# Kernel optimization log

Hardware: AMD Instinct MI355X
Metric: run time of the kernel (lower is better)

Reference implementation:

```python
import jax, jax.numpy as jnp
import numpy as np

B, N, M = 32, 512, 512
EPS = 0.05        # Sinkhorn entropic regularization (approximates exact EMD flow)
N_ITERS = 50      # fixed Sinkhorn iterations
NEG = -1e9        # log(0) surrogate for masked particles


def setup_inputs() -> dict:
    key = jax.random.key(0)
    k1, k2, k3, k4, k5, k6 = jax.random.split(key, 6)
    a_mask = (jax.random.uniform(k1, (B, N)) > 0.1).astype(jnp.float32)
    b_mask = (jax.random.uniform(k2, (B, M)) > 0.1).astype(jnp.float32)
    a_mask = a_mask.at[:, 0].set(1.0)  # guarantee nonempty clouds
    b_mask = b_mask.at[:, 0].set(1.0)
    pc_a = jnp.concatenate([jax.random.normal(k3, (B, N, 2)),
                            jax.random.uniform(k5, (B, N, 1), minval=0.1, maxval=1.0)], axis=-1)
    pc_b = jnp.concatenate([jax.random.normal(k4, (B, M, 2)),
                            jax.random.uniform(k6, (B, M, 1), minval=0.1, maxval=1.0)], axis=-1)
    return {"a_mask": a_mask, "pc_a": pc_a, "b_mask": b_mask, "pc_b": pc_b}


def _sinkhorn_logflow(loga, logb, logK):
    # log-domain Sinkhorn: find P with row sums exp(loga), col sums exp(logb)
    def body(i, carry):
        logu, logv = carry
        logu = loga - jax.scipy.special.logsumexp(logK + logv[:, None, :], axis=2)
        logv = logb - jax.scipy.special.logsumexp(logK + logu[:, :, None], axis=1)
        return (logu, logv)
    logu = jnp.zeros_like(loga)
    logv = jnp.zeros_like(logb)
    logu, logv = jax.lax.fori_loop(0, N_ITERS, body, (logu, logv))
    return logu[:, :, None] + logK + logv[:, None, :]  # [B, N, M]


def _emd_flow(a_pt, b_pt, dist, va, vb):
    # normalized pt distributions (emd(..., norm=True))
    aw = a_pt / jnp.sum(a_pt, axis=-1, keepdims=True)
    bw = b_pt / jnp.sum(b_pt, axis=-1, keepdims=True)
    loga = jnp.where(va, jnp.log(jnp.where(va, aw, 1.0)), NEG)
    logb = jnp.where(vb, jnp.log(jnp.where(vb, bw, 1.0)), NEG)
    logK = -dist / EPS
    flow = jnp.exp(_sinkhorn_logflow(loga, logb, logK))
    return flow * va[:, :, None].astype(flow.dtype) * vb[:, None, :].astype(flow.dtype)


def reference(a_mask, pc_a, b_mask, pc_b):
    a_pt = a_mask * pc_a[..., -1]              # [B, N]
    b_pt = b_mask * pc_b[..., -1]              # [B, M]
    va = a_pt > 0
    vb = b_pt > 0
    # masked pairwise (eta, phi) distance matrix
    diff = pc_a[:, :, None, :2] - pc_b[:, None, :, :2]      # [B, N, M, 2]
    d = jnp.sqrt(jnp.sum(diff * diff, axis=-1) + 1e-12)
    dist = d * va[:, :, None].astype(d.dtype) * vb[:, None, :].astype(d.dtype)
    # optimal-transport flow (detached in the original: computed on CPU numpy)
    flow = jax.lax.stop_gradient(_emd_flow(a_pt, b_pt, dist, va, vb))
    ot_term = jnp.sum(dist * dist * flow, axis=(-1, -2))    # [B]
    # huber_loss(reduction='none'), delta=1
    e = a_pt.sum(axis=-1) - b_pt.sum(axis=-1)
    huber = jnp.where(jnp.abs(e) <= 1.0, 0.5 * e * e, jnp.abs(e) - 0.5)
    return ot_term + huber
```

## Files before the change

kernel.cpp:

```cpp
#include <hip/hip_runtime.h>
#include <math.h>

#define NB 32
#define NP 512
#define RG 8
#define RPB 64
#define ITERS 50
#define EPSV   0.05f
#define INVEPS 20.0f

typedef unsigned long long u64;
typedef unsigned int u32;

#define N_PACK (2*NB*RG*NP)

__device__ __forceinline__ void st32(u32* p, u32 v) {
  __hip_atomic_store(p, v, __ATOMIC_RELAXED, __HIP_MEMORY_SCOPE_AGENT);
}
__device__ __forceinline__ u32 ld32(const u32* p) {
  return __hip_atomic_load(p, __ATOMIC_RELAXED, __HIP_MEMORY_SCOPE_AGENT);
}
__device__ __forceinline__ void st64f(float2* p, float tag, float val) {
  union { float2 f; u64 u; } c; c.f = make_float2(tag, val);
  __hip_atomic_store((u64*)p, c.u, __ATOMIC_RELAXED, __HIP_MEMORY_SCOPE_AGENT);
}
__device__ __forceinline__ float2 ld64f(const float2* p) {
  union { u64 u; float2 f; } c;
  c.u = __hip_atomic_load((const u64*)p, __ATOMIC_RELAXED, __HIP_MEMORY_SCOPE_AGENT);
  return c.f;
}

__device__ __forceinline__ u32 tag_of(int k) {
  return (0x765431u >> (4 * (k % 6))) & 0xFu;
}
__device__ __forceinline__ u32 pack_slot(float v, u32 tag) {
  return (__float_as_uint(v) & ~7u) | tag;
}

__global__ __launch_bounds__(NP) void emd_kernel(
    const float* __restrict__ a_mask, const float* __restrict__ pc_a,
    const float* __restrict__ b_mask, const float* __restrict__ pc_b,
    u32* __restrict__ pack, float2* __restrict__ epi,
    float* __restrict__ out)
{
  const int rb = blockIdx.x;
  const int b  = rb >> 3;
  const int rg = rb & 7;
  const int t  = threadIdx.x;
  const int chunk = t & 7;
  const int lrow  = t >> 3;
  const int grow  = rg*RPB + lrow;
  const int lane  = t & 63, wid = t >> 6;

  __shared__ __align__(16) float rho_l[NP];
  __shared__ __align__(16) float bw_l[NP];
  __shared__ __align__(16) float u_l[RPB];
  __shared__ __align__(16) float sm[NP];
  __shared__ float red[16];

  float4 eKreg[16];
  float  eKcol[RPB];
  float  aw_r, bw_t, hub = 0.f;

  {
    const float apt = a_mask[b*NP+t] * pc_a[((size_t)b*NP+t)*3+2];
    const float bpt = b_mask[b*NP+t] * pc_b[((size_t)b*NP+t)*3+2];
    float ra = apt, rv = bpt;
    #pragma unroll
    for (int o = 32; o; o >>= 1) { ra += __shfl_xor(ra, o); rv += __shfl_xor(rv, o); }
    if (lane == 0) { red[wid] = ra; red[8+wid] = rv; }
    __syncthreads();
    float asum = 0.f, bsum = 0.f;
    #pragma unroll
    for (int w = 0; w < 8; ++w) { asum += red[w]; bsum += red[8+w]; }
    const float e = asum - bsum, ae = fabsf(e);
    hub = (ae <= 1.f) ? 0.5f*e*e : (ae - 0.5f);
    sm[t]   = (apt > 0.f) ? apt/asum : 0.f;
    bw_l[t] = (bpt > 0.f) ? bpt/bsum : 0.f;
    __syncthreads();
    aw_r = sm[grow];
    bw_t = bw_l[t];
    const float ax = pc_a[((size_t)b*NP+grow)*3+0];
    const float ay = pc_a[((size_t)b*NP+grow)*3+1];
    const bool  va = aw_r > 0.f;
    #pragma unroll
    for (int cc = 0; cc < 16; ++cc) {
      float r[4];
      #pragma unroll
      for (int e2 = 0; e2 < 4; ++e2) {
        const int col = 32*cc + 4*chunk + e2;
        const float bx = pc_b[((size_t)b*NP+col)*3+0];
        const float by = pc_b[((size_t)b*NP+col)*3+1];
        const bool  vb = bw_l[col] > 0.f;
        const float dx = ax-bx, dy = ay-by;
        const float d  = sqrtf(dx*dx + dy*dy + 1e-12f);
        r[e2] = (va && vb) ? __expf((-INVEPS)*d) : 1.f;
      }
      eKreg[cc] = make_float4(r[0], r[1], r[2], r[3]);
    }
    const float bx0 = pc_b[((size_t)b*NP+t)*3+0];
    const float by0 = pc_b[((size_t)b*NP+t)*3+1];
    const bool  vb0 = bw_t > 0.f;
    #pragma unroll
    for (int i = 0; i < RPB; ++i) {
      const int row = rg*RPB + i;
      const float axi = pc_a[((size_t)b*NP+row)*3+0];
      const float ayi = pc_a[((size_t)b*NP+row)*3+1];
      const bool  vai = sm[row] > 0.f;
      const float dx = axi-bx0, dy = ayi-by0;
      const float d  = sqrtf(dx*dx + dy*dy + 1e-12f);
      eKcol[i] = (vai && vb0) ? __expf((-INVEPS)*d) : 1.f;
    }
    rho_l[t] = 1.f;
    __syncthreads();
  }

  for (int k = 1; k <= ITERS; ++k) {
    const u32 tag = tag_of(k);
    const int par = k & 1;
    const u32* base = pack + ((size_t)par*NB + b)*RG*NP + t;

    {
      const float4* r4p = (const float4*)rho_l;
      float dot = 0.f;
      #pragma unroll
      for (int cc = 0; cc < 16; ++cc) {
        const float4 g4 = r4p[8*cc + chunk];
        const float4 kk = eKreg[cc];
        dot += kk.x*g4.x + kk.y*g4.y + kk.z*g4.z + kk.w*g4.w;
      }
      #pragma unroll
      for (int o = 4; o; o >>= 1) dot += __shfl_xor(dot, o);
      if (chunk == 0) u_l[lrow] = aw_r / fmaxf(dot, 1e-38f);
    }
    __syncthreads();

    float sc_own;
    {
      const float4* u4p = (const float4*)u_l;
      float sc = 0.f;
      #pragma unroll
      for (int i4 = 0; i4 < 16; ++i4) {
        const float4 uu = u4p[i4];
        sc += eKcol[4*i4+0]*uu.x + eKcol[4*i4+1]*uu.y
            + eKcol[4*i4+2]*uu.z + eKcol[4*i4+3]*uu.w;
      }
      sc_own = sc;
      st32(pack + (((size_t)par*NB + b)*RG + rg)*NP + t, pack_slot(sc, tag));
    }

    u32 q[RG];
    #pragma unroll
    for (int r = 0; r < RG; ++r)
      if (r != rg) q[r] = ld32(base + (size_t)r*NP);

    {
      unsigned pend = 0xFFu & ~(1u << rg);
      long long sweeps = 0;
      while (true) {
        unsigned np = 0;
        #pragma unroll
        for (int r = 0; r < RG; ++r)
          if ((pend >> r) & 1u)
            if ((q[r] & 7u) != tag) np |= (1u << r);
        pend = np;
        if (!pend) break;
        #pragma unroll
        for (int r = 0; r < RG; ++r)
          if ((pend >> r) & 1u)
            q[r] = ld32(base + (size_t)r*NP);
        if (++sweeps > (1LL<<24)) break;
      }
      float S = sc_own;
      #pragma unroll
      for (int r = 0; r < RG; ++r)
        if (r != rg) S += __uint_as_float(q[r]);
      rho_l[t] = bw_t / fmaxf(S, 1e-38f);
    }
    __syncthreads();
  }

  float acc = 0.f;
  {
    const float ur = u_l[lrow];
    const float4* r4p = (const float4*)rho_l;
    #pragma unroll
    for (int cc = 0; cc < 16; ++cc) {
      const float4 g4 = r4p[8*cc + chunk];
      const float4 kk = eKreg[cc];
      const float ek[4] = {kk.x, kk.y, kk.z, kk.w};
      const float vv[4] = {g4.x, g4.y, g4.z, g4.w};
      #pragma unroll
      for (int e2 = 0; e2 < 4; ++e2) {
        const float lk = __logf(fmaxf(ek[e2], 1e-38f));
        const float d2 = (EPSV*lk)*(EPSV*lk);
        const float v  = d2 * ur * ek[e2] * vv[e2];
        acc += (ek[e2] > 0.f) ? v : 0.f;
      }
    }
  }
  sm[t] = acc;
  __syncthreads();
  if (t < 64) {
    float v = 0.f;
    #pragma unroll
    for (int q2 = 0; q2 < 8; ++q2) v += sm[t*8+q2];
    #pragma unroll
    for (int o = 32; o; o >>= 1) v += __shfl_xor(v, o);
    if (t == 0) st64f(epi + (size_t)b*RG + rg, 51.f, v);
  }
  if (rg == 0 && t < RG) {
    float2 pr;
    long long spins = 0;
    do {
      pr = ld64f(epi + (size_t)b*RG + t);
      if (pr.x == 51.f) break;
      __builtin_amdgcn_s_sleep(1);
    } while (++spins < (1LL<<27));
    float v = pr.y;
    #pragma unroll
    for (int o = 4; o; o >>= 1) v += __shfl_xor(v, o);
    if (t == 0) out[b] = v + hub;
  }
}

extern "C" void kernel_launch(void* const* d_in, const int* in_sizes, int n_in,
                              void* d_out, int out_size, void* d_ws, size_t ws_size,
                              hipStream_t stream) {
  const float* a_mask = (const float*)d_in[0];
  const float* pc_a   = (const float*)d_in[1];
  const float* b_mask = (const float*)d_in[2];
  const float* pc_b   = (const float*)d_in[3];
  float* out = (float*)d_out;
  u32*    pack = (u32*)d_ws;
  float2* epi  = (float2*)(pack + N_PACK);
  (void)in_sizes; (void)n_in; (void)out_size; (void)ws_size;

  emd_kernel<<<NB*RG, NP, 0, stream>>>(a_mask, pc_a, b_mask, pc_b,
                                       pack, epi, out);
}
```

Before: 196.1 us.

## Process two batches per block with 16 row groups to overlap cross-block exchange

Adds a new kernel in which each block handles two batch elements (X and Y) interleaved, with each batch split across 16 blocks of 32 rows instead of 8 blocks of 64. The Y half's compute is issued while the X half's cross-block partial sums are in flight, hiding the spin-wait latency of the inter-block reduction. Spin loops also add s_sleep backoff. The old kernel is kept as a fallback when the workspace is too small. Twice as many exchange partners per batch raises the polling traffic, and the extra register arrays may cause spilling.

```diff
diff --git a/kernel.cpp b/kernel.cpp
--- a/kernel.cpp
+++ b/kernel.cpp
@@ -3,16 +3,21 @@
 
 #define NB 32
 #define NP 512
-#define RG 8
-#define RPB 64
 #define ITERS 50
 #define EPSV   0.05f
 #define INVEPS 20.0f
 
+#define NPAIR 16
+#define GG 16
+#define RPB2 32
+#define PAR_STRIDE2 (NPAIR*2*GG*NP)
+#define N_PACK2 (2*PAR_STRIDE2)
+#define RG 8
+#define RPB 64
+#define N_PACK (2*NB*RG*NP)
+
 typedef unsigned long long u64;
 typedef unsigned int u32;
-
-#define N_PACK (2*NB*RG*NP)
 
 __device__ __forceinline__ void st32(u32* p, u32 v) {
   __hip_atomic_store(p, v, __ATOMIC_RELAXED, __HIP_MEMORY_SCOPE_AGENT);
@@ -37,7 +42,335 @@
   return (__float_as_uint(v) & ~7u) | tag;
 }
 
-__global__ __launch_bounds__(NP) void emd_kernel(
+__global__ __launch_bounds__(NP, 2) void emd_pair_kernel(
+    const float* __restrict__ a_mask, const float* __restrict__ pc_a,
+    const float* __restrict__ b_mask, const float* __restrict__ pc_b,
+    u32* __restrict__ pack, float2* __restrict__ epi,
+    float* __restrict__ out)
+{
+  const int rb = blockIdx.x;
+  const int p  = rb >> 4;
+  const int g  = rb & 15;
+  const int X  = 2*p, Y = 2*p + 1;
+  const int t  = threadIdx.x;
+  const int chunk = t & 15;
+  const int lrow  = t >> 4;
+  const int grow  = g*RPB2 + lrow;
+  const int lane  = t & 63, wid = t >> 6;
+
+  __shared__ __align__(16) float rhoX_l[NP], rhoY_l[NP];
+  __shared__ __align__(16) float bwX_l[NP],  bwY_l[NP];
+  __shared__ __align__(16) float uX_l[RPB2], uY_l[RPB2];
+  __shared__ __align__(16) float sm[NP];
+  __shared__ float red[32];
+
+  float4 eKregX[8], eKregY[8];
+  float  eKcolX[RPB2], eKcolY[RPB2];
+  float  aw_rX, bw_tX, hubX;
+  float  aw_rY, bw_tY, hubY;
+
+  u32* ownX = pack + ((size_t)(X*GG + g))*NP + t;
+  u32* ownY = pack + ((size_t)(Y*GG + g))*NP + t;
+  const u32* baseX = pack + (size_t)X*GG*NP + t;
+  const u32* baseY = pack + (size_t)Y*GG*NP + t;
+
+  const float aptX = a_mask[X*NP+t] * pc_a[((size_t)X*NP+t)*3+2];
+  const float bptX = b_mask[X*NP+t] * pc_b[((size_t)X*NP+t)*3+2];
+  const float aptY = a_mask[Y*NP+t] * pc_a[((size_t)Y*NP+t)*3+2];
+  const float bptY = b_mask[Y*NP+t] * pc_b[((size_t)Y*NP+t)*3+2];
+  {
+    float r0 = aptX, r1 = bptX, r2 = aptY, r3 = bptY;
+    #pragma unroll
+    for (int o = 32; o; o >>= 1) {
+      r0 += __shfl_xor(r0, o); r1 += __shfl_xor(r1, o);
+      r2 += __shfl_xor(r2, o); r3 += __shfl_xor(r3, o);
+    }
+    if (lane == 0) { red[wid]=r0; red[8+wid]=r1; red[16+wid]=r2; red[24+wid]=r3; }
+    __syncthreads();
+    float asX=0.f, bsX=0.f, asY=0.f, bsY=0.f;
+    #pragma unroll
+    for (int w = 0; w < 8; ++w) {
+      asX += red[w]; bsX += red[8+w]; asY += red[16+w]; bsY += red[24+w];
+    }
+    const float eX = asX - bsX, aeX = fabsf(eX);
+    hubX = (aeX <= 1.f) ? 0.5f*eX*eX : (aeX - 0.5f);
+    const float eY = asY - bsY, aeY = fabsf(eY);
+    hubY = (aeY <= 1.f) ? 0.5f*eY*eY : (aeY - 0.5f);
+    sm[t]    = (aptX > 0.f) ? aptX/asX : 0.f;
+    bwX_l[t] = (bptX > 0.f) ? bptX/bsX : 0.f;
+    bwY_l[t] = (bptY > 0.f) ? bptY/bsY : 0.f;
+    __syncthreads();
+    aw_rX = sm[grow]; bw_tX = bwX_l[t]; bw_tY = bwY_l[t];
+    {
+      const float ax = pc_a[((size_t)X*NP+grow)*3+0];
+      const float ay = pc_a[((size_t)X*NP+grow)*3+1];
+      const bool  va = aw_rX > 0.f;
+      #pragma unroll
+      for (int cc = 0; cc < 8; ++cc) {
+        float r[4];
+        #pragma unroll
+        for (int e2 = 0; e2 < 4; ++e2) {
+          const int col = 64*cc + 4*chunk + e2;
+          const float bx = pc_b[((size_t)X*NP+col)*3+0];
+          const float by = pc_b[((size_t)X*NP+col)*3+1];
+          const bool  vb = bwX_l[col] > 0.f;
+          const float dx = ax-bx, dy = ay-by;
+          const float d  = sqrtf(dx*dx + dy*dy + 1e-12f);
+          r[e2] = (va && vb) ? __expf((-INVEPS)*d) : 1.f;
+        }
+        eKregX[cc] = make_float4(r[0], r[1], r[2], r[3]);
+      }
+      const float bx0 = pc_b[((size_t)X*NP+t)*3+0];
+      const float by0 = pc_b[((size_t)X*NP+t)*3+1];
+      const bool  vb0 = bw_tX > 0.f;
+      #pragma unroll
+      for (int i = 0; i < RPB2; ++i) {
+        const int row = g*RPB2 + i;
+        const float axi = pc_a[((size_t)X*NP+row)*3+0];
+        const float ayi = pc_a[((size_t)X*NP+row)*3+1];
+        const bool  vai = sm[row] > 0.f;
+        const float dx = axi-bx0, dy = ayi-by0;
+        const float d  = sqrtf(dx*dx + dy*dy + 1e-12f);
+        eKcolX[i] = (vai && vb0) ? __expf((-INVEPS)*d) : 1.f;
+      }
+    }
+    rhoX_l[t] = 1.f;
+    __syncthreads();
+    sm[t] = (aptY > 0.f) ? aptY/asY : 0.f;
+    __syncthreads();
+    aw_rY = sm[grow];
+    {
+      const float ax = pc_a[((size_t)Y*NP+grow)*3+0];
+      const float ay = pc_a[((size_t)Y*NP+grow)*3+1];
+      const bool  va = aw_rY > 0.f;
+      #pragma unroll
+      for (int cc = 0; cc < 8; ++cc) {
+        float r[4];
+        #pragma unroll
+        for (int e2 = 0; e2 < 4; ++e2) {
+          const int col = 64*cc + 4*chunk + e2;
+          const float bx = pc_b[((size_t)Y*NP+col)*3+0];
+          const float by = pc_b[((size_t)Y*NP+col)*3+1];
+          const bool  vb = bwY_l[col] > 0.f;
+          const float dx = ax-bx, dy = ay-by;
+          const float d  = sqrtf(dx*dx + dy*dy + 1e-12f);
+          r[e2] = (va && vb) ? __expf((-INVEPS)*d) : 1.f;
+        }
+        eKregY[cc] = make_float4(r[0], r[1], r[2], r[3]);
+      }
+      const float bx0 = pc_b[((size_t)Y*NP+t)*3+0];
+      const float by0 = pc_b[((size_t)Y*NP+t)*3+1];
+      const bool  vb0 = bw_tY > 0.f;
+      #pragma unroll
+      for (int i = 0; i < RPB2; ++i) {
+        const int row = g*RPB2 + i;
+        const float axi = pc_a[((size_t)Y*NP+row)*3+0];
+        const float ayi = pc_a[((size_t)Y*NP+row)*3+1];
+        const bool  vai = sm[row] > 0.f;
+        const float dx = axi-bx0, dy = ayi-by0;
+        const float d  = sqrtf(dx*dx + dy*dy + 1e-12f);
+        eKcolY[i] = (vai && vb0) ? __expf((-INVEPS)*d) : 1.f;
+      }
+    }
+    rhoY_l[t] = 1.f;
+    __syncthreads();
+  }
+
+  for (int k = 1; k <= ITERS; ++k) {
+    const u32 tag = tag_of(k);
+    const size_t po = (size_t)(k & 1) * (size_t)PAR_STRIDE2;
+
+    {
+      const float4* r4p = (const float4*)rhoX_l;
+      float dot = 0.f;
+      #pragma unroll
+      for (int cc = 0; cc < 8; ++cc) {
+        const float4 g4 = r4p[16*cc + chunk];
+        const float4 kk = eKregX[cc];
+        dot += kk.x*g4.x + kk.y*g4.y + kk.z*g4.z + kk.w*g4.w;
+      }
+      #pragma unroll
+      for (int o = 8; o; o >>= 1) dot += __shfl_xor(dot, o);
+      if (chunk == 0) uX_l[lrow] = aw_rX / fmaxf(dot, 1e-38f);
+    }
+    __syncthreads();
+
+    float scoX;
+    {
+      const float4* u4p = (const float4*)uX_l;
+      float sc = 0.f;
+      #pragma unroll
+      for (int i4 = 0; i4 < 8; ++i4) {
+        const float4 uu = u4p[i4];
+        sc += eKcolX[4*i4+0]*uu.x + eKcolX[4*i4+1]*uu.y
+            + eKcolX[4*i4+2]*uu.z + eKcolX[4*i4+3]*uu.w;
+      }
+      scoX = sc;
+      st32(ownX + po, pack_slot(sc, tag));
+    }
+    u32 qx[GG];
+    #pragma unroll
+    for (int r = 0; r < GG; ++r)
+      if (r != g) qx[r] = ld32(baseX + po + (size_t)r*NP);
+    asm volatile("" ::: "memory");
+
+    {
+      const float4* r4p = (const float4*)rhoY_l;
+      float dot = 0.f;
+      #pragma unroll
+      for (int cc = 0; cc < 8; ++cc) {
+        const float4 g4 = r4p[16*cc + chunk];
+        const float4 kk = eKregY[cc];
+        dot += kk.x*g4.x + kk.y*g4.y + kk.z*g4.z + kk.w*g4.w;
+      }
+      #pragma unroll
+      for (int o = 8; o; o >>= 1) dot += __shfl_xor(dot, o);
+      if (chunk == 0) uY_l[lrow] = aw_rY / fmaxf(dot, 1e-38f);
+    }
+    __syncthreads();
+
+    float scoY;
+    {
+      const float4* u4p = (const float4*)uY_l;
+      float sc = 0.f;
+      #pragma unroll
+      for (int i4 = 0; i4 < 8; ++i4) {
+        const float4 uu = u4p[i4];
+        sc += eKcolY[4*i4+0]*uu.x + eKcolY[4*i4+1]*uu.y
+            + eKcolY[4*i4+2]*uu.z + eKcolY[4*i4+3]*uu.w;
+      }
+      scoY = sc;
+      st32(ownY + po, pack_slot(sc, tag));
+    }
+    u32 qy[GG];
+    #pragma unroll
+    for (int r = 0; r < GG; ++r)
+      if (r != g) qy[r] = ld32(baseY + po + (size_t)r*NP);
+    asm volatile("" ::: "memory");
+
+    {
+      unsigned pend = 0xFFFFu & ~(1u << g);
+      int sweeps = 0;
+      while (true) {
+        unsigned np = 0;
+        #pragma unroll
+        for (int r = 0; r < GG; ++r)
+          if ((pend >> r) & 1u)
+            if ((qx[r] & 7u) != tag) np |= (1u << r);
+        pend = np;
+        if (!pend) break;
+        #pragma unroll
+        for (int r = 0; r < GG; ++r)
+          if ((pend >> r) & 1u)
+            qx[r] = ld32(baseX + po + (size_t)r*NP);
+        ++sweeps;
+        if (sweeps > 64) __builtin_amdgcn_s_sleep(1);
+        if (sweeps > (1<<16)) break;
+      }
+      float S = scoX;
+      #pragma unroll
+      for (int r = 0; r < GG; ++r)
+        if (r != g) S += __uint_as_float(qx[r]);
+      rhoX_l[t] = bw_tX / fmaxf(S, 1e-38f);
+    }
+
+    {
+      unsigned pend = 0xFFFFu & ~(1u << g);
+      int sweeps = 0;
+      while (true) {
+        unsigned np = 0;
+        #pragma unroll
+        for (int r = 0; r < GG; ++r)
+          if ((pend >> r) & 1u)
+            if ((qy[r] & 7u) != tag) np |= (1u << r);
+        pend = np;
+        if (!pend) break;
+        #pragma unroll
+        for (int r = 0; r < GG; ++r)
+          if ((pend >> r) & 1u)
+            qy[r] = ld32(baseY + po + (size_t)r*NP);
+        ++sweeps;
+        if (sweeps > 64) __builtin_amdgcn_s_sleep(1);
+        if (sweeps > (1<<16)) break;
+      }
+      float S = scoY;
+      #pragma unroll
+      for (int r = 0; r < GG; ++r)
+        if (r != g) S += __uint_as_float(qy[r]);
+      rhoY_l[t] = bw_tY / fmaxf(S, 1e-38f);
+    }
+    __syncthreads();
+  }
+
+  float accX = 0.f, accY = 0.f;
+  {
+    const float urX = uX_l[lrow];
+    const float4* r4p = (const float4*)rhoX_l;
+    #pragma unroll
+    for (int cc = 0; cc < 8; ++cc) {
+      const float4 g4 = r4p[16*cc + chunk];
+      const float4 kk = eKregX[cc];
+      const float ek[4] = {kk.x, kk.y, kk.z, kk.w};
+      const float vv[4] = {g4.x, g4.y, g4.z, g4.w};
+      #pragma unroll
+      for (int e2 = 0; e2 < 4; ++e2) {
+        const float lk = __logf(fmaxf(ek[e2], 1e-38f));
+        const float d2 = (EPSV*lk)*(EPSV*lk);
+        const float v  = d2 * urX * ek[e2] * vv[e2];
+        accX += (ek[e2] > 0.f) ? v : 0.f;
+      }
+    }
+  }
+  {
+    const float urY = uY_l[lrow];
+    const float4* r4p = (const float4*)rhoY_l;
+    #pragma unroll
+    for (int cc = 0; cc < 8; ++cc) {
+      const float4 g4 = r4p[16*cc + chunk];
+      const float4 kk = eKregY[cc];
+      const float ek[4] = {kk.x, kk.y, kk.z, kk.w};
+      const float vv[4] = {g4.x, g4.y, g4.z, g4.w};
+      #pragma unroll
+      for (int e2 = 0; e2 < 4; ++e2) {
+        const float lk = __logf(fmaxf(ek[e2], 1e-38f));
+        const float d2 = (EPSV*lk)*(EPSV*lk);
+        const float v  = d2 * urY * ek[e2] * vv[e2];
+        accY += (ek[e2] > 0.f) ? v : 0.f;
+      }
+    }
+  }
+  sm[t] = accX; bwX_l[t] = accY;
+  __syncthreads();
+  if (t < 64) {
+    float vX = 0.f, vY = 0.f;
+    #pragma unroll
+    for (int q2 = 0; q2 < 8; ++q2) { vX += sm[t*8+q2]; vY += bwX_l[t*8+q2]; }
+    #pragma unroll
+    for (int o = 32; o; o >>= 1) { vX += __shfl_xor(vX, o); vY += __shfl_xor(vY, o); }
+    if (t == 0) {
+      st64f(epi + (size_t)X*GG + g, 51.f, vX);
+      st64f(epi + (size_t)Y*GG + g, 51.f, vY);
+    }
+  }
+  if (g == 0 && t < 2*GG) {
+    const int bxl = t >> 4;
+    const int gg  = t & 15;
+    const float2* ep = epi + (size_t)(X + bxl)*GG + gg;
+    float2 pr;
+    long long spins = 0;
+    do {
+      pr = ld64f(ep);
+      if (pr.x == 51.f) break;
+      __builtin_amdgcn_s_sleep(1);
+    } while (++spins < (1LL<<24));
+    float v = pr.y;
+    #pragma unroll
+    for (int o = 8; o; o >>= 1) v += __shfl_xor(v, o);
+    if (gg == 0) out[X + bxl] = v + (bxl ? hubY : hubX);
+  }
+}
+
+__global__ __launch_bounds__(NP) void emd_kernel_r7(
     const float* __restrict__ a_mask, const float* __restrict__ pc_a,
     const float* __restrict__ b_mask, const float* __restrict__ pc_b,
     u32* __restrict__ pack, float2* __restrict__ epi,
@@ -119,7 +452,6 @@
     const u32 tag = tag_of(k);
     const int par = k & 1;
     const u32* base = pack + ((size_t)par*NB + b)*RG*NP + t;
-
     {
       const float4* r4p = (const float4*)rho_l;
       float dot = 0.f;
@@ -134,7 +466,6 @@
       if (chunk == 0) u_l[lrow] = aw_r / fmaxf(dot, 1e-38f);
     }
     __syncthreads();
-
     float sc_own;
     {
       const float4* u4p = (const float4*)u_l;
@@ -148,12 +479,10 @@
       sc_own = sc;
       st32(pack + (((size_t)par*NB + b)*RG + rg)*NP + t, pack_slot(sc, tag));
     }
-
     u32 q[RG];
     #pragma unroll
     for (int r = 0; r < RG; ++r)
       if (r != rg) q[r] = ld32(base + (size_t)r*NP);
-
     {
       unsigned pend = 0xFFu & ~(1u << rg);
       long long sweeps = 0;
@@ -169,7 +498,7 @@
         for (int r = 0; r < RG; ++r)
           if ((pend >> r) & 1u)
             q[r] = ld32(base + (size_t)r*NP);
-        if (++sweeps > (1LL<<24)) break;
+        if (++sweeps > (1LL<<22)) break;
       }
       float S = sc_own;
       #pragma unroll
@@ -216,7 +545,7 @@
       pr = ld64f(epi + (size_t)b*RG + t);
       if (pr.x == 51.f) break;
       __builtin_amdgcn_s_sleep(1);
-    } while (++spins < (1LL<<27));
+    } while (++spins < (1LL<<24));
     float v = pr.y;
     #pragma unroll
     for (int o = 4; o; o >>= 1) v += __shfl_xor(v, o);
@@ -232,10 +561,17 @@
   const float* b_mask = (const float*)d_in[2];
   const float* pc_b   = (const float*)d_in[3];
   float* out = (float*)d_out;
-  u32*    pack = (u32*)d_ws;
-  float2* epi  = (float2*)(pack + N_PACK);
-  (void)in_sizes; (void)n_in; (void)out_size; (void)ws_size;
-
-  emd_kernel<<<NB*RG, NP, 0, stream>>>(a_mask, pc_a, b_mask, pc_b,
-                                       pack, epi, out);
-}
+  u32* pack = (u32*)d_ws;
+  (void)in_sizes; (void)n_in; (void)out_size;
+
+  const size_t need_pair = (size_t)N_PACK2*4 + (size_t)NB*GG*sizeof(float2);
+  if (ws_size >= need_pair) {
+    float2* epi = (float2*)(pack + N_PACK2);
+    emd_pair_kernel<<<NPAIR*GG, NP, 0, stream>>>(a_mask, pc_a, b_mask, pc_b,
+                                                 pack, epi, out);
+  } else {
+    float2* epi = (float2*)(pack + N_PACK);
+    emd_kernel_r7<<<NB*RG, NP, 0, stream>>>(a_mask, pc_a, b_mask, pc_b,
+                                            pack, epi, out);
+  }
+}
```

After: 357.8 us. 82.4% more time.
